# Kernel optimization log

Measured on AMD Instinct MI355X. Metric: run time of the kernel, lower is better.

## Reference

```python
import jax, jax.numpy as jnp
import numpy as np

CODEBOOK_SIZE = 8192
LATENT_DIM = 256
BETA = 0.25        # commitment_beta
DECAY = 0.99       # ema_decay
EPS = 1e-5         # ema_eps
DIVERSITY_WEIGHT = 1.0


def _hadamard(n):
    # Sylvester construction; n must be a power of 2 (scipy.linalg.hadamard equivalent)
    H = np.array([[1.0]], dtype=np.float32)
    while H.shape[0] < n:
        H = np.block([[H, H], [H, -H]])
    return H


def setup_inputs() -> dict:
    key = jax.random.key(0)
    k1, k2, k3 = jax.random.split(key, 3)
    B, C, Hh, Ww = 16, LATENT_DIM, 32, 32
    lim = 1.0 / CODEBOOK_SIZE
    x = jax.random.normal(k1, (B, C, Hh, Ww), dtype=jnp.float32)
    embedding_weight = jax.random.uniform(k2, (CODEBOOK_SIZE, LATENT_DIM), jnp.float32, -lim, lim)
    rotation_matrix = jnp.asarray(_hadamard(LATENT_DIM))
    ema_cluster_size = jnp.ones((CODEBOOK_SIZE,), jnp.float32)
    ema_w = jax.random.uniform(k3, (CODEBOOK_SIZE, LATENT_DIM), jnp.float32, -lim, lim)
    return {
        "x": x,
        "embedding_weight": embedding_weight,
        "rotation_matrix": rotation_matrix,
        "ema_cluster_size": ema_cluster_size,
        "ema_w": ema_w,
    }


def reference(x, embedding_weight, rotation_matrix, ema_cluster_size, ema_w):
    B, C, H, W = x.shape
    K = embedding_weight.shape[0]
    N = B * H * W

    # (B,C,H,W) -> (N, D)
    x_flat = jnp.transpose(x, (0, 2, 3, 1)).reshape(N, C)
    x_rot = x_flat @ rotation_matrix                     # (N, D)

    # squared-distance cdist: ||xr||^2 + ||e||^2 - 2 xr e^T  -> (N, K)
    distances = (
        jnp.sum(x_rot * x_rot, axis=-1, keepdims=True)
        + jnp.sum(embedding_weight * embedding_weight, axis=-1)[None, :]
        - 2.0 * (x_rot @ embedding_weight.T)
    )
    encoding_indices = jnp.argmin(distances, axis=-1)    # (N,) int

    # gather-based quantized output (== one-hot @ embedding)
    quant_flat = jnp.take(embedding_weight, encoding_indices, axis=0)  # (N, D)
    quant_out = jnp.transpose(quant_flat.reshape(B, H, W, C), (0, 3, 1, 2))

    sg = jax.lax.stop_gradient
    commitment_loss = BETA * jnp.mean((sg(quant_out) - x) ** 2)
    codebook_loss = jnp.mean((quant_out - sg(x)) ** 2)

    # avg one-hot probabilities via scatter-add (== encodings.mean(0))
    counts = jnp.zeros((K,), x.dtype).at[encoding_indices].add(1.0)
    avg_probs = counts / N
    entropy_loss = -jnp.sum(avg_probs * jnp.log(avg_probs + 1e-10)) * DIVERSITY_WEIGHT
    perplexity = jnp.exp(entropy_loss)

    # EMA codebook update (training path; buffers, no grad)
    new_cluster = ema_cluster_size * DECAY + (1.0 - DECAY) * counts
    n_tot = jnp.sum(new_cluster)
    new_cluster = (new_cluster + EPS) / (n_tot + K * EPS) * n_tot
    # dw = encodings^T @ x_rotated  == segment-sum of x_rot by code index
    dw = jnp.zeros((K, C), x.dtype).at[encoding_indices].add(x_rot)
    new_ema_w = ema_w * DECAY + (1.0 - DECAY) * dw
    new_embedding = new_ema_w / new_cluster[:, None]

    # straight-through estimator
    quant_out_st = x + sg(quant_out - x)

    return (
        quant_out_st,
        codebook_loss,
        commitment_loss,
        entropy_loss,
        perplexity,
        encoding_indices,
        new_embedding,
        new_ema_w,
        new_cluster,
    )
```

## Files before the change

kernel.cpp:

```cpp
#include <hip/hip_runtime.h>
#include <hip/hip_bf16.h>


typedef unsigned long long u64;
typedef unsigned int u32;
typedef unsigned short ushortv;
typedef __attribute__((ext_vector_type(8))) short short8;
typedef __attribute__((ext_vector_type(4))) float f32x4;
typedef __attribute__((ext_vector_type(4))) unsigned short ushort4v;

#define CAP    128
#define MARGIN 0.012f

__device__ inline ushortv f2bf(float f) {
    u32 u = __float_as_uint(f);
    u32 r = (u + 0x7fffu + ((u >> 16) & 1u)) >> 16;
    return (ushortv)r;
}
__device__ inline float bf2f(ushortv h) { return __uint_as_float((u32)h << 16); }

__device__ inline void fwht_row(const float* __restrict__ x, int n, int l,
                                float& v0, float& v1, float& v2, float& v3) {
    int b = n >> 10, hw = n & 1023;
    const float* xp = x + (size_t)b * 262144 + hw;
    v0 = xp[(size_t)(l)       * 1024];
    v1 = xp[(size_t)(l + 64)  * 1024];
    v2 = xp[(size_t)(l + 128) * 1024];
    v3 = xp[(size_t)(l + 192) * 1024];
    float a0 = v0 + v2, a2 = v0 - v2;
    float a1 = v1 + v3, a3 = v1 - v3;
    v0 = a0 + a1; v1 = a0 - a1; v2 = a2 + a3; v3 = a2 - a3;
    #pragma unroll
    for (int s = 32; s >= 1; s >>= 1) {
        float o0 = __shfl_xor(v0, s, 64);
        float o1 = __shfl_xor(v1, s, 64);
        float o2 = __shfl_xor(v2, s, 64);
        float o3 = __shfl_xor(v3, s, 64);
        bool hi = (l & s) != 0;
        v0 = hi ? (o0 - v0) : (v0 + o0);
        v1 = hi ? (o1 - v1) : (v1 + o1);
        v2 = hi ? (o2 - v2) : (v2 + o2);
        v3 = hi ? (o3 - v3) : (v3 + o3);
    }
}

__global__ void k1_split(const float* __restrict__ x,
                         char* __restrict__ Ap,
                         float* __restrict__ An) {
    int t = threadIdx.x, wid = t >> 6, l = t & 63;
    int n = blockIdx.x * 4 + wid;
    float v0, v1, v2, v3;
    fwht_row(x, n, l, v0, v1, v2, v3);
    int rr = n & 15;
    char* tp = Ap + (size_t)(n >> 4) * 8192 + rr * 64;
    int sw = (rr >> 1) & 3;
    float vv[4] = {v0, v1, v2, v3};
    #pragma unroll
    for (int r = 0; r < 4; ++r) {
        ushortv h = f2bf(vv[r]);
        float pv = __shfl_down(vv[r], 1, 64);
        if (!(l & 1)) {
            u32 w = (u32)h | ((u32)f2bf(pv) << 16);
            int c = r * 2 + (l >> 5);
            int s = (l >> 3) & 3;
            *(u32*)(tp + c * 1024 + ((s ^ sw) * 16) + (l & 7) * 2) = w;
        }
    }
    float sq = v0*v0 + v1*v1 + v2*v2 + v3*v3;
    #pragma unroll
    for (int s = 32; s >= 1; s >>= 1) sq += __shfl_xor(sq, s, 64);
    if (l == 0) An[n] = sq;
}

__global__ void k1b_esplit(const float* __restrict__ E, char* __restrict__ Bp) {
    int g = blockIdx.x * 256 + threadIdx.x;
    int row = g >> 6, c4 = g & 63;
    float4 e = *(const float4*)&E[(size_t)row * 256 + c4 * 4];
    ushort4v eh = (ushort4v){f2bf(e.x), f2bf(e.y), f2bf(e.z), f2bf(e.w)};
    int rr = row & 15;
    int c = c4 >> 3;
    int s = (c4 >> 1) & 3;
    int sw = (rr >> 1) & 3;
    *(ushort4v*)(Bp + (size_t)(row >> 4) * 8192 + c * 1024 + rr * 64
                 + ((s ^ sw) * 16) + (c4 & 1) * 8) = eh;
}

__global__ __launch_bounds__(256, 2)
void k2_mfma(const char* __restrict__ Ap, const char* __restrict__ Bp,
             const float* __restrict__ An,
             u64* __restrict__ rowkey, u32* __restrict__ cnt,
             u64* __restrict__ cand) {
    __shared__ __align__(16) char AsB[2][8192];
    __shared__ __align__(16) char BsB[2][8192];
    __shared__ u64 wavemin[2][128];
    __shared__ float thr[128];
    __shared__ float nrm[128];
    int t = threadIdx.x;
    int l = t & 63, wid = t >> 6;
    int wr = wid & 1, wc = wid >> 1;
    int rb = blockIdx.x * 128, kb = blockIdx.y * 128;
    if (t < 128) nrm[t] = An[rb + t];

    f32x4 acc[4][4];
    #pragma unroll
    for (int i = 0; i < 4; ++i)
        #pragma unroll
        for (int j = 0; j < 4; ++j) acc[i][j] = (f32x4){0.f, 0.f, 0.f, 0.f};

    int i0 = wid * 2, i1 = wid * 2 + 1;
    const char* aT0 = Ap + ((size_t)(rb >> 4) + i0) * 8192 + (size_t)l * 16;
    const char* aT1 = Ap + ((size_t)(rb >> 4) + i1) * 8192 + (size_t)l * 16;
    const char* bT0 = Bp + ((size_t)(kb >> 4) + i0) * 8192 + (size_t)l * 16;
    const char* bT1 = Bp + ((size_t)(kb >> 4) + i1) * 8192 + (size_t)l * 16;

#define STAGE(kc, buf) do {                                                    \
    int off_ = (kc) * 1024;                                                    \
    __builtin_amdgcn_global_load_lds(                                          \
        (const __attribute__((address_space(1))) u32*)(aT0 + off_),            \
        (__attribute__((address_space(3))) u32*)(AsB[buf] + i0 * 1024), 16, 0, 0); \
    __builtin_amdgcn_global_load_lds(                                          \
        (const __attribute__((address_space(1))) u32*)(aT1 + off_),            \
        (__attribute__((address_space(3))) u32*)(AsB[buf] + i1 * 1024), 16, 0, 0); \
    __builtin_amdgcn_global_load_lds(                                          \
        (const __attribute__((address_space(1))) u32*)(bT0 + off_),            \
        (__attribute__((address_space(3))) u32*)(BsB[buf] + i0 * 1024), 16, 0, 0); \
    __builtin_amdgcn_global_load_lds(                                          \
        (const __attribute__((address_space(1))) u32*)(bT1 + off_),            \
        (__attribute__((address_space(3))) u32*)(BsB[buf] + i1 * 1024), 16, 0, 0); \
} while (0)

    STAGE(0, 0);
    __syncthreads();
    #pragma unroll
    for (int kc = 0; kc < 8; ++kc) {
        int cb = kc & 1;
        if (kc < 7) STAGE(kc + 1, cb ^ 1);
        short8 afr[4], bfr[4];
        #pragma unroll
        for (int f = 0; f < 4; ++f) {
            int row = wr * 64 + f * 16 + (l & 15);
            int kgp = (l >> 4) ^ ((row >> 1) & 3);
            afr[f] = *(const short8*)(AsB[cb] + row * 64 + kgp * 16);
            int col = wc * 64 + f * 16 + (l & 15);
            int kgq = (l >> 4) ^ ((col >> 1) & 3);
            bfr[f] = *(const short8*)(BsB[cb] + col * 64 + kgq * 16);
        }
        #pragma unroll
        for (int fi = 0; fi < 4; ++fi)
            #pragma unroll
            for (int fj = 0; fj < 4; ++fj)
                acc[fi][fj] = __builtin_amdgcn_mfma_f32_16x16x32_bf16(
                    afr[fi], bfr[fj], acc[fi][fj], 0, 0, 0);
        __syncthreads();
    }
#undef STAGE

    #pragma unroll
    for (int fi = 0; fi < 4; ++fi) {
        #pragma unroll
        for (int j = 0; j < 4; ++j) {
            int rt = wr * 64 + fi * 16 + (l >> 4) * 4 + j;
            float a = nrm[rt];
            u64 m = ~0ull;
            #pragma unroll
            for (int fj = 0; fj < 4; ++fj) {
                int col = kb + wc * 64 + fj * 16 + (l & 15);
                float dv = a - 2.0f * acc[fi][fj][j];
                u64 key = ((u64)__float_as_uint(dv) << 32) | (u32)col;
                m = key < m ? key : m;
            }
            #pragma unroll
            for (int s = 1; s <= 8; s <<= 1) {
                u64 o = __shfl_xor(m, s, 64);
                m = o < m ? o : m;
            }
            if ((l & 15) == 0) wavemin[wc][rt] = m;
        }
    }
    __syncthreads();
    if (t < 128) {
        u64 m0 = wavemin[0][t], m1 = wavemin[1][t];
        u64 m = m0 < m1 ? m0 : m1;
        u64 old = atomicMin(&rowkey[rb + t], m);
        u64 cur = old < m ? old : m;
        thr[t] = __uint_as_float((u32)(cur >> 32)) + MARGIN;
    }
    __syncthreads();
    #pragma unroll
    for (int fi = 0; fi < 4; ++fi)
        #pragma unroll
        for (int fj = 0; fj < 4; ++fj)
            #pragma unroll
            for (int j = 0; j < 4; ++j) {
                int rt = wr * 64 + fi * 16 + (l >> 4) * 4 + j;
                float dv = nrm[rt] - 2.0f * acc[fi][fj][j];
                if (dv < thr[rt]) {
                    int col = kb + wc * 64 + fj * 16 + (l & 15);
                    int r = rb + rt;
                    u32 pos = atomicAdd(&cnt[r], 1u);
                    if (pos < CAP)
                        cand[(size_t)r * CAP + pos] =
                            ((u64)__float_as_uint(dv) << 32) | (u32)col;
                }
            }
}

__global__ void k_refine(const float* __restrict__ x, const float* __restrict__ E,
                         const float* __restrict__ An, const u64* __restrict__ rowkey,
                         const u32* __restrict__ cnt, const u64* __restrict__ cand,
                         int* __restrict__ idx, float* __restrict__ out5,
                         float* __restrict__ counts, float* __restrict__ dw) {
    int t = threadIdx.x, wid = t >> 6, l = t & 63;
    int n = blockIdx.x * 4 + wid;
    float v0, v1, v2, v3;
    fwht_row(x, n, l, v0, v1, v2, v3);
    float a = An[n];
    float mdv = __uint_as_float((u32)(rowkey[n] >> 32)) + MARGIN;
    u32 c = cnt[n];
    u64 best = ~0ull;
    if (c <= CAP) {
        for (u32 i = 0; i < c; ++i) {
            u64 ck = cand[(size_t)n * CAP + i];
            if (__uint_as_float((u32)(ck >> 32)) > mdv) continue;
            int k = (int)(ck & 0xffffffffu);
            const float* e = E + (size_t)k * 256;
            float p = v0 * e[l];
            p = fmaf(v1, e[64 + l], p);
            p = fmaf(v2, e[128 + l], p);
            p = fmaf(v3, e[192 + l], p);
            #pragma unroll
            for (int s = 1; s <= 32; s <<= 1) p += __shfl_xor(p, s, 64);
            float dv = a - 2.0f * p;
            u64 key = ((u64)__float_as_uint(dv) << 32) | (u32)k;
            best = key < best ? key : best;
        }
    } else {
        for (int k = 0; k < 8192; ++k) {
            const float* e = E + (size_t)k * 256;
            float p = v0 * e[l];
            p = fmaf(v1, e[64 + l], p);
            p = fmaf(v2, e[128 + l], p);
            p = fmaf(v3, e[192 + l], p);
            #pragma unroll
            for (int s = 1; s <= 32; s <<= 1) p += __shfl_xor(p, s, 64);
            float dv = a - 2.0f * p;
            u64 key = ((u64)__float_as_uint(dv) << 32) | (u32)k;
            best = key < best ? key : best;
        }
    }
    int k = (int)(best & 0xffffffffu);
    if (l == 0) {
        idx[n] = k;
        out5[n] = (float)k;
        atomicAdd(&counts[k], 1.0f);
    }
    size_t db = (size_t)k * 256;
    atomicAdd(&dw[db + l],       v0);
    atomicAdd(&dw[db + 64 + l],  v1);
    atomicAdd(&dw[db + 128 + l], v2);
    atomicAdd(&dw[db + 192 + l], v3);
}

__global__ void k4c_quant(const float* __restrict__ x,
                          const float* __restrict__ E,
                          const int* __restrict__ idx,
                          float* __restrict__ out0,
                          float* __restrict__ sse) {
    int t = threadIdx.x;
    int o4 = blockIdx.x * 256 + t;
    int o = o4 * 4;
    int c = (o >> 10) & 255;
    int b = o >> 18;
    int n0 = b * 1024 + ((o >> 5) & 31) * 32 + (o & 31);
    int4 id4 = *(const int4*)&idx[n0];
    float4 xv = *(const float4*)&x[o];
    float q0 = E[(size_t)id4.x * 256 + c];
    float q1 = E[(size_t)id4.y * 256 + c];
    float q2 = E[(size_t)id4.z * 256 + c];
    float q3 = E[(size_t)id4.w * 256 + c];
    float d0 = q0 - xv.x, d1 = q1 - xv.y, d2 = q2 - xv.z, d3 = q3 - xv.w;
    float4 r;
    r.x = xv.x + d0; r.y = xv.y + d1; r.z = xv.z + d2; r.w = xv.w + d3;
    *(float4*)&out0[o] = r;
    float s = d0*d0 + d1*d1 + d2*d2 + d3*d3;
    #pragma unroll
    for (int sh = 32; sh >= 1; sh >>= 1) s += __shfl_xor(s, sh, 64);
    __shared__ float ps[4];
    if ((t & 63) == 0) ps[t >> 6] = s;
    __syncthreads();
    if (t == 0) atomicAdd(sse, ps[0] + ps[1] + ps[2] + ps[3]);
}

__global__ void k5_scalars(const float* __restrict__ counts,
                           const float* __restrict__ cs,
                           const float* __restrict__ sse,
                           float* __restrict__ out_sc,
                           float* __restrict__ out8) {
    __shared__ float r1[1024], r2[1024];
    __shared__ float ntot_s;
    int t = threadIdx.x;
    float snc = 0.0f, sent = 0.0f;
    #pragma unroll
    for (int j = 0; j < 8; ++j) {
        int k = t + 1024 * j;
        float cnt_ = counts[k];
        float nc = cs[k] * 0.99f + 0.01f * cnt_;
        snc += nc;
        float p = cnt_ * (1.0f / 16384.0f);
        sent += p * logf(p + 1e-10f);
    }
    r1[t] = snc; r2[t] = sent;
    __syncthreads();
    for (int sh = 512; sh >= 1; sh >>= 1) {
        if (t < sh) { r1[t] += r1[t + sh]; r2[t] += r2[t + sh]; }
        __syncthreads();
    }
    if (t == 0) {
        float n_tot = r1[0];
        ntot_s = n_tot;
        float ent = -r2[0];
        float cb = sse[0] * (1.0f / 4194304.0f);
        out_sc[0] = cb;
        out_sc[1] = 0.25f * cb;
        out_sc[2] = ent;
        out_sc[3] = expf(ent);
    }
    __syncthreads();
    float n_tot = ntot_s;
    #pragma unroll
    for (int j = 0; j < 8; ++j) {
        int k = t + 1024 * j;
        float cnt_ = counts[k];
        float nc = cs[k] * 0.99f + 0.01f * cnt_;
        out8[k] = (nc + 1e-5f) / (n_tot + 0.08192f) * n_tot;
    }
}

__global__ void k6_ema(const float* __restrict__ dw,
                       const float* __restrict__ ema_w,
                       const float* __restrict__ ncl,
                       float* __restrict__ out6,
                       float* __restrict__ out7) {
    int f4 = blockIdx.x * 256 + threadIdx.x;
    int f = f4 * 4;
    int k = f >> 8;
    float4 d = *(const float4*)&dw[f];
    float4 wv = *(const float4*)&ema_w[f];
    float4 nw;
    nw.x = wv.x * 0.99f + 0.01f * d.x;
    nw.y = wv.y * 0.99f + 0.01f * d.y;
    nw.z = wv.z * 0.99f + 0.01f * d.z;
    nw.w = wv.w * 0.99f + 0.01f * d.w;
    *(float4*)&out7[f] = nw;
    float c = ncl[k];
    float4 e;
    e.x = nw.x / c; e.y = nw.y / c; e.z = nw.z / c; e.w = nw.w / c;
    *(float4*)&out6[f] = e;
}

extern "C" void kernel_launch(void* const* d_in, const int* in_sizes, int n_in,
                              void* d_out, int out_size, void* d_ws, size_t ws_size,
                              hipStream_t stream) {
    const float* x     = (const float*)d_in[0];
    const float* E     = (const float*)d_in[1];
    const float* cs    = (const float*)d_in[3];
    const float* ema_w = (const float*)d_in[4];
    float* out = (float*)d_out;

    char* ws = (char*)d_ws;
    char*  Ap     = ws;
    char*  Bp     = ws + 8388608;
    float* An     = (float*)(ws + 12582912);
    u64*   rowkey = (u64*)  (ws + 12648448);
    u32*   cnt    = (u32*)  (ws + 12779520);
    u64*   cand   = (u64*)  (ws + 12845056);
    int*   idxb   = (int*)  (ws + 29622272);
    float* counts = (float*)(ws + 29687808);
    float* dw     = (float*)(ws + 29720576);
    float* sse    = (float*)(ws + 38109184);

    hipMemsetAsync(rowkey, 0xFF, 16384 * 8, stream);
    hipMemsetAsync(cnt, 0, 16384 * 4, stream);
    hipMemsetAsync(counts, 0, 8192 * 4, stream);
    hipMemsetAsync(dw, 0, 8388608, stream);
    hipMemsetAsync(sse, 0, 256, stream);

    k1_split<<<4096, 256, 0, stream>>>(x, Ap, An);
    k1b_esplit<<<2048, 256, 0, stream>>>(E, Bp);
    k2_mfma<<<dim3(128, 64), 256, 0, stream>>>(Ap, Bp, An, rowkey, cnt, cand);
    k_refine<<<4096, 256, 0, stream>>>(x, E, An, rowkey, cnt, cand,
                                       idxb, out + 4194308, counts, dw);
    k4c_quant<<<4096, 256, 0, stream>>>(x, E, idxb, out, sse);
    k5_scalars<<<1, 1024, 0, stream>>>(counts, cs, sse, out + 4194304, out + 8404996);
    k6_ema<<<2048, 256, 0, stream>>>(dw, ema_w, out + 8404996,
                                     out + 4210692, out + 6307844);
}
```

Measured before the change: 381.4 us.

## Cache rotated rows, fold memsets into kernels, restage quantize through LDS, halve CAP

k1_split now writes the fp32 rotated rows to a workspace buffer and initializes rowkey and cnt itself, which removes two memsets. k_refine reads the cached rows with float4 loads instead of recomputing the transform from strided x, and it also reads E rows as float4. The quantize kernel now gathers 64 codebook rows into LDS and writes coalesced output across fewer blocks. The workspace is reorganized so dw aliases the Ap buffer, and CAP drops to 64, which raises the chance that a row overflows into the full 8192-entry scan.

```diff
diff --git a/kernel.cpp b/kernel.cpp
--- a/kernel.cpp
+++ b/kernel.cpp
@@ -9,7 +9,7 @@
 typedef __attribute__((ext_vector_type(4))) float f32x4;
 typedef __attribute__((ext_vector_type(4))) unsigned short ushort4v;
 
-#define CAP    128
+#define CAP    64
 #define MARGIN 0.012f
 
 __device__ inline ushortv f2bf(float f) {
@@ -17,7 +17,6 @@
     u32 r = (u + 0x7fffu + ((u >> 16) & 1u)) >> 16;
     return (ushortv)r;
 }
-__device__ inline float bf2f(ushortv h) { return __uint_as_float((u32)h << 16); }
 
 __device__ inline void fwht_row(const float* __restrict__ x, int n, int l,
                                 float& v0, float& v1, float& v2, float& v3) {
@@ -46,11 +45,19 @@
 
 __global__ void k1_split(const float* __restrict__ x,
                          char* __restrict__ Ap,
-                         float* __restrict__ An) {
+                         float* __restrict__ xrot,
+                         float* __restrict__ An,
+                         u64* __restrict__ rowkey,
+                         u32* __restrict__ cnt) {
     int t = threadIdx.x, wid = t >> 6, l = t & 63;
     int n = blockIdx.x * 4 + wid;
     float v0, v1, v2, v3;
     fwht_row(x, n, l, v0, v1, v2, v3);
+    float* xr = xrot + (size_t)n * 256;
+    xr[l]       = v0;
+    xr[64 + l]  = v1;
+    xr[128 + l] = v2;
+    xr[192 + l] = v3;
     int rr = n & 15;
     char* tp = Ap + (size_t)(n >> 4) * 8192 + rr * 64;
     int sw = (rr >> 1) & 3;
@@ -69,7 +76,11 @@
     float sq = v0*v0 + v1*v1 + v2*v2 + v3*v3;
     #pragma unroll
     for (int s = 32; s >= 1; s >>= 1) sq += __shfl_xor(sq, s, 64);
-    if (l == 0) An[n] = sq;
+    if (l == 0) {
+        An[n] = sq;
+        rowkey[n] = ~0ull;
+        cnt[n] = 0u;
+    }
 }
 
 __global__ void k1b_esplit(const float* __restrict__ E, char* __restrict__ Bp) {
@@ -205,15 +216,14 @@
             }
 }
 
-__global__ void k_refine(const float* __restrict__ x, const float* __restrict__ E,
+__global__ void k_refine(const float* __restrict__ xrot, const float* __restrict__ E,
                          const float* __restrict__ An, const u64* __restrict__ rowkey,
                          const u32* __restrict__ cnt, const u64* __restrict__ cand,
                          int* __restrict__ idx, float* __restrict__ out5,
                          float* __restrict__ counts, float* __restrict__ dw) {
     int t = threadIdx.x, wid = t >> 6, l = t & 63;
     int n = blockIdx.x * 4 + wid;
-    float v0, v1, v2, v3;
-    fwht_row(x, n, l, v0, v1, v2, v3);
+    float4 xv = *(const float4*)&xrot[(size_t)n * 256 + 4 * l];
     float a = An[n];
     float mdv = __uint_as_float((u32)(rowkey[n] >> 32)) + MARGIN;
     u32 c = cnt[n];
@@ -223,11 +233,11 @@
             u64 ck = cand[(size_t)n * CAP + i];
             if (__uint_as_float((u32)(ck >> 32)) > mdv) continue;
             int k = (int)(ck & 0xffffffffu);
-            const float* e = E + (size_t)k * 256;
-            float p = v0 * e[l];
-            p = fmaf(v1, e[64 + l], p);
-            p = fmaf(v2, e[128 + l], p);
-            p = fmaf(v3, e[192 + l], p);
+            float4 ev = *(const float4*)&E[(size_t)k * 256 + 4 * l];
+            float p = xv.x * ev.x;
+            p = fmaf(xv.y, ev.y, p);
+            p = fmaf(xv.z, ev.z, p);
+            p = fmaf(xv.w, ev.w, p);
             #pragma unroll
             for (int s = 1; s <= 32; s <<= 1) p += __shfl_xor(p, s, 64);
             float dv = a - 2.0f * p;
@@ -236,11 +246,11 @@
         }
     } else {
         for (int k = 0; k < 8192; ++k) {
-            const float* e = E + (size_t)k * 256;
-            float p = v0 * e[l];
-            p = fmaf(v1, e[64 + l], p);
-            p = fmaf(v2, e[128 + l], p);
-            p = fmaf(v3, e[192 + l], p);
+            float4 ev = *(const float4*)&E[(size_t)k * 256 + 4 * l];
+            float p = xv.x * ev.x;
+            p = fmaf(xv.y, ev.y, p);
+            p = fmaf(xv.z, ev.z, p);
+            p = fmaf(xv.w, ev.w, p);
             #pragma unroll
             for (int s = 1; s <= 32; s <<= 1) p += __shfl_xor(p, s, 64);
             float dv = a - 2.0f * p;
@@ -254,39 +264,50 @@
         out5[n] = (float)k;
         atomicAdd(&counts[k], 1.0f);
     }
-    size_t db = (size_t)k * 256;
-    atomicAdd(&dw[db + l],       v0);
-    atomicAdd(&dw[db + 64 + l],  v1);
-    atomicAdd(&dw[db + 128 + l], v2);
-    atomicAdd(&dw[db + 192 + l], v3);
-}
-
-__global__ void k4c_quant(const float* __restrict__ x,
-                          const float* __restrict__ E,
-                          const int* __restrict__ idx,
-                          float* __restrict__ out0,
-                          float* __restrict__ sse) {
-    int t = threadIdx.x;
-    int o4 = blockIdx.x * 256 + t;
-    int o = o4 * 4;
-    int c = (o >> 10) & 255;
-    int b = o >> 18;
-    int n0 = b * 1024 + ((o >> 5) & 31) * 32 + (o & 31);
-    int4 id4 = *(const int4*)&idx[n0];
-    float4 xv = *(const float4*)&x[o];
-    float q0 = E[(size_t)id4.x * 256 + c];
-    float q1 = E[(size_t)id4.y * 256 + c];
-    float q2 = E[(size_t)id4.z * 256 + c];
-    float q3 = E[(size_t)id4.w * 256 + c];
-    float d0 = q0 - xv.x, d1 = q1 - xv.y, d2 = q2 - xv.z, d3 = q3 - xv.w;
-    float4 r;
-    r.x = xv.x + d0; r.y = xv.y + d1; r.z = xv.z + d2; r.w = xv.w + d3;
-    *(float4*)&out0[o] = r;
-    float s = d0*d0 + d1*d1 + d2*d2 + d3*d3;
-    #pragma unroll
-    for (int sh = 32; sh >= 1; sh >>= 1) s += __shfl_xor(s, sh, 64);
+    size_t db = (size_t)k * 256 + 4 * l;
+    atomicAdd(&dw[db + 0], xv.x);
+    atomicAdd(&dw[db + 1], xv.y);
+    atomicAdd(&dw[db + 2], xv.z);
+    atomicAdd(&dw[db + 3], xv.w);
+}
+
+__global__ __launch_bounds__(256, 2)
+void k4c_quant(const float* __restrict__ x,
+               const float* __restrict__ E,
+               const int* __restrict__ idx,
+               float* __restrict__ out0,
+               float* __restrict__ sse) {
+    __shared__ float Q[64][257];
     __shared__ float ps[4];
-    if ((t & 63) == 0) ps[t >> 6] = s;
+    int t = threadIdx.x, wid = t >> 6, l = t & 63;
+    int n0 = blockIdx.x * 64;
+    int b = n0 >> 10, hw0 = n0 & 1023;
+    #pragma unroll 4
+    for (int tt = wid * 16; tt < wid * 16 + 16; ++tt) {
+        int k = idx[n0 + tt];
+        float4 e = *(const float4*)&E[(size_t)k * 256 + 4 * l];
+        Q[tt][4*l + 0] = e.x; Q[tt][4*l + 1] = e.y;
+        Q[tt][4*l + 2] = e.z; Q[tt][4*l + 3] = e.w;
+    }
+    __syncthreads();
+    float sacc = 0.f;
+    int hwl = 4 * (l & 15);
+    #pragma unroll 4
+    for (int j = 0; j < 16; ++j) {
+        int c = wid * 64 + j * 4 + (l >> 4);
+        size_t o = (size_t)b * 262144 + (size_t)c * 1024 + hw0 + hwl;
+        float4 xv = *(const float4*)&x[o];
+        float q0 = Q[hwl + 0][c], q1 = Q[hwl + 1][c];
+        float q2 = Q[hwl + 2][c], q3 = Q[hwl + 3][c];
+        float d0 = q0 - xv.x, d1 = q1 - xv.y, d2 = q2 - xv.z, d3 = q3 - xv.w;
+        float4 r;
+        r.x = xv.x + d0; r.y = xv.y + d1; r.z = xv.z + d2; r.w = xv.w + d3;
+        *(float4*)&out0[o] = r;
+        sacc += d0*d0 + d1*d1 + d2*d2 + d3*d3;
+    }
+    #pragma unroll
+    for (int sh = 32; sh >= 1; sh >>= 1) sacc += __shfl_xor(sacc, sh, 64);
+    if (l == 0) ps[wid] = sacc;
     __syncthreads();
     if (t == 0) atomicAdd(sse, ps[0] + ps[1] + ps[2] + ps[3]);
 }
@@ -369,28 +390,26 @@
 
     char* ws = (char*)d_ws;
     char*  Ap     = ws;
+    float* dw     = (float*)ws;
     char*  Bp     = ws + 8388608;
-    float* An     = (float*)(ws + 12582912);
-    u64*   rowkey = (u64*)  (ws + 12648448);
-    u32*   cnt    = (u32*)  (ws + 12779520);
-    u64*   cand   = (u64*)  (ws + 12845056);
-    int*   idxb   = (int*)  (ws + 29622272);
-    float* counts = (float*)(ws + 29687808);
-    float* dw     = (float*)(ws + 29720576);
-    float* sse    = (float*)(ws + 38109184);
-
-    hipMemsetAsync(rowkey, 0xFF, 16384 * 8, stream);
-    hipMemsetAsync(cnt, 0, 16384 * 4, stream);
-    hipMemsetAsync(counts, 0, 8192 * 4, stream);
-    hipMemsetAsync(dw, 0, 8388608, stream);
-    hipMemsetAsync(sse, 0, 256, stream);
-
-    k1_split<<<4096, 256, 0, stream>>>(x, Ap, An);
+    int*   idxb   = (int*)  (ws + 8388608);
+    float* counts = (float*)(ws + 8454144);
+    float* sse    = (float*)(ws + 8486912);
+    float* xrot   = (float*)(ws + 12582912);
+    float* An     = (float*)(ws + 29360128);
+    u64*   rowkey = (u64*)  (ws + 29425664);
+    u32*   cnt    = (u32*)  (ws + 29556736);
+    u64*   cand   = (u64*)  (ws + 29622272);
+
+    k1_split<<<4096, 256, 0, stream>>>(x, Ap, xrot, An, rowkey, cnt);
     k1b_esplit<<<2048, 256, 0, stream>>>(E, Bp);
     k2_mfma<<<dim3(128, 64), 256, 0, stream>>>(Ap, Bp, An, rowkey, cnt, cand);
-    k_refine<<<4096, 256, 0, stream>>>(x, E, An, rowkey, cnt, cand,
+    hipMemsetAsync(dw, 0, 8388608, stream);
+    hipMemsetAsync(counts, 0, 8192 * 4, stream);
+    hipMemsetAsync(sse, 0, 256, stream);
+    k_refine<<<4096, 256, 0, stream>>>(xrot, E, An, rowkey, cnt, cand,
                                        idxb, out + 4194308, counts, dw);
-    k4c_quant<<<4096, 256, 0, stream>>>(x, E, idxb, out, sse);
+    k4c_quant<<<256, 256, 0, stream>>>(x, E, idxb, out, sse);
     k5_scalars<<<1, 1024, 0, stream>>>(counts, cs, sse, out + 4194304, out + 8404996);
     k6_ema<<<2048, 256, 0, stream>>>(dw, ema_w, out + 8404996,
                                      out + 4210692, out + 6307844);
```

Measured after the change: 362.0 us. -5.1%, faster.
